# Kernel optimization log

Measured on AMD Instinct MI355X. Metric: run time of the kernel, lower is better.

The kernel has to match this reference:

```python
import jax, jax.numpy as jnp
import numpy as np

F = 128   # num_features
H = 128   # hidden sizes
U = 128   # u_size == out_size
N = 50000
E = 600000
B = 64
L = 4     # hops + 1 layers


def _scatter_mean(vals, idx, num_segments):
    s = jax.ops.segment_sum(vals, idx, num_segments=num_segments)
    cnt = jax.ops.segment_sum(jnp.ones((vals.shape[0],), vals.dtype), idx,
                              num_segments=num_segments)
    return s / jnp.maximum(cnt, 1.0)[:, None]


def setup_inputs() -> dict:
    key = jax.random.key(0)
    ks = jax.random.split(key, 20)
    x = jax.random.normal(ks[0], (N, F), jnp.float32)
    edge_index = jax.random.randint(ks[1], (2, E), 0, N, jnp.int64)
    u = jax.random.normal(ks[2], (B, U), jnp.float32)
    batch = jnp.sort(jax.random.randint(ks[3], (N,), 0, B, jnp.int64))
    sc = 0.05
    # stacked per-layer params (all layer dims identical since u_size==out_size)
    params = {
        'n1w1': jax.random.normal(ks[4], (L, F, H), jnp.float32) * sc,
        'n1b1': jnp.zeros((L, H), jnp.float32),
        'n1w2': jax.random.normal(ks[5], (L, H, H), jnp.float32) * sc,
        'n1b2': jnp.zeros((L, H), jnp.float32),
        'n2w1': jax.random.normal(ks[6], (L, F + H + U, H), jnp.float32) * sc,
        'n2b1': jnp.zeros((L, H), jnp.float32),
        'n2w2': jax.random.normal(ks[7], (L, H, F), jnp.float32) * sc,
        'n2b2': jnp.zeros((L, F), jnp.float32),
        'gw1': jax.random.normal(ks[8], (L, F + U, H), jnp.float32) * sc,
        'gb1': jnp.zeros((L, H), jnp.float32),
        'gw2': jax.random.normal(ks[9], (L, H, U), jnp.float32) * sc,
        'gb2': jnp.zeros((L, U), jnp.float32),
    }
    return dict(x=x, edge_index=edge_index, u=u, batch=batch, **params)


def reference(x, edge_index, u, batch,
              n1w1, n1b1, n1w2, n1b2, n2w1, n2b1, n2w2, n2b2,
              gw1, gb1, gw2, gb2):
    row, col = edge_index[0], edge_index[1]
    for l in range(L):
        # NodeModel
        m = jax.nn.relu(x[row] @ n1w1[l] + n1b1[l]) @ n1w2[l] + n1b2[l]  # [E,H]
        agg = _scatter_mean(m, col, N)                                    # [N,H]
        h = jnp.concatenate([x, agg, u[batch]], axis=1)                   # [N,F+H+U]
        x = jax.nn.relu(h @ n2w1[l] + n2b1[l]) @ n2w2[l] + n2b2[l]        # [N,F]
        # GlobalModel (uses updated x)
        g = jnp.concatenate([u, _scatter_mean(x, batch, B)], axis=1)      # [B,F+U]
        u = jax.nn.relu(g @ gw1[l] + gb1[l]) @ gw2[l] + gb2[l]            # [B,U]
    return (x, u)
```

## Files before the change

kernel.cpp:

```cpp
#include <hip/hip_runtime.h>

typedef __bf16 bf16;
typedef bf16 bf16x8 __attribute__((ext_vector_type(8)));
typedef bf16 bf16x4 __attribute__((ext_vector_type(4)));
typedef float floatx4 __attribute__((ext_vector_type(4)));

#define MFMA __builtin_amdgcn_mfma_f32_16x16x32_bf16


__global__ void hist_kernel(const int* __restrict__ ei, int* __restrict__ cnt, int E) {
  int e = blockIdx.x * blockDim.x + threadIdx.x;
  if (e < E) atomicAdd(&cnt[ei[E + e]], 1);
}

__global__ void gcnt_kernel(const int* __restrict__ batch, int* __restrict__ gcnt,
                            int N, int B) {
  const int b = threadIdx.x;
  if (b >= B) return;
  auto lb = [&](int v) {
    int lo = 0, hi = N;
    while (lo < hi) {
      const int mid = (lo + hi) >> 1;
      if (batch[mid] < v) lo = mid + 1; else hi = mid;
    }
    return lo;
  };
  gcnt[b] = lb(b + 1) - lb(b);
}

__global__ void scan1_kernel(const int* __restrict__ cnt, int* __restrict__ colptr,
                             int* __restrict__ rctr, int* __restrict__ btot, int n) {
  __shared__ int sd[256];
  const int tid = threadIdx.x;
  const int i0 = blockIdx.x * 2048 + tid * 8;
  int v[8];
  int tot = 0;
#pragma unroll
  for (int j = 0; j < 8; ++j) {
    const int i = i0 + j;
    v[j] = (i < n) ? cnt[i] : 0;
    tot += v[j];
  }
  sd[tid] = tot;
  __syncthreads();
  for (int off = 1; off < 256; off <<= 1) {
    const int t = (tid >= off) ? sd[tid - off] : 0;
    __syncthreads();
    sd[tid] += t;
    __syncthreads();
  }
  int excl = sd[tid] - tot;
#pragma unroll
  for (int j = 0; j < 8; ++j) {
    const int i = i0 + j;
    if (i < n) { colptr[i] = excl; rctr[i] = excl; }
    excl += v[j];
  }
  if (tid == 255) btot[blockIdx.x] = sd[255];
}

__global__ void scan2_kernel(int* __restrict__ colptr, int* __restrict__ rctr,
                             const int* __restrict__ btot, int n) {
  __shared__ int off_s;
  const int tid = threadIdx.x;
  if (blockIdx.x == 0) return;
  if (tid == 0) {
    int o = 0;
    for (int j = 0; j < (int)blockIdx.x; ++j) o += btot[j];
    off_s = o;
  }
  __syncthreads();
  const int off = off_s;
  const int i0 = blockIdx.x * 2048 + tid * 8;
#pragma unroll
  for (int j = 0; j < 8; ++j) {
    const int i = i0 + j;
    if (i < n) { colptr[i] += off; rctr[i] += off; }
  }
}

__global__ void place_kernel(const int* __restrict__ ei, int* __restrict__ rctr,
                             int* __restrict__ esrow, int E) {
  int e = blockIdx.x * blockDim.x + threadIdx.x;
  if (e >= E) return;
  const int r = ei[e];
  const int c = ei[E + e];
  const int p = atomicAdd(&rctr[c], 1);
  esrow[p] = r;
}

__global__ void wsplit_kernel(const float* __restrict__ src, bf16* __restrict__ dst,
                              int Ksrc, int K, int HH) {
  const int l = blockIdx.y;
  const int gid = blockIdx.x * blockDim.x + threadIdx.x;
  if (gid >= K * HH) return;
  const int h = gid / K, k = gid - h * K;
  const float v = src[(size_t)l * Ksrc * HH + (size_t)k * HH + h];
  const bf16 hi = (bf16)v;
  const bf16 lo = (bf16)(v - (float)hi);
  bf16* d = dst + (size_t)l * 2 * K * HH;
  d[(size_t)h * K + k] = hi;
  d[(size_t)K * HH + (size_t)h * K + k] = lo;
}

__global__ void xsplit_kernel(const float* __restrict__ x, bf16* __restrict__ xhi,
                              bf16* __restrict__ xlo, int n4) {
  const int i = blockIdx.x * 256 + threadIdx.x;
  if (i >= n4) return;
  const float4 v = ((const float4*)x)[i];
  bf16x4 h, l;
  const float vv[4] = {v.x, v.y, v.z, v.w};
#pragma unroll
  for (int r = 0; r < 4; ++r) {
    h[r] = (bf16)vv[r];
    l[r] = (bf16)(vv[r] - (float)h[r]);
  }
  *(bf16x4*)&xhi[(size_t)i * 4] = h;
  *(bf16x4*)&xlo[(size_t)i * 4] = l;
}

__global__ __launch_bounds__(256, 4)
void pnode_mfma(const bf16* __restrict__ xh, const bf16* __restrict__ xl,
                const bf16* __restrict__ w1t, const float* __restrict__ b1,
                const bf16* __restrict__ w2t, const float* __restrict__ b2,
                bf16* __restrict__ P, int N) {
  __shared__ __align__(16) bf16 R[2 * 64 * 136];

  const int tid = threadIdx.x;
  const int n0 = blockIdx.x * 64;
  const int wave = tid >> 6, lane = tid & 63, q = lane >> 4, lr = lane & 15;
  const int hbase = wave * 32;

  int nn[4];
#pragma unroll
  for (int nt = 0; nt < 4; ++nt) {
    int n = n0 + nt * 16 + lr;
    nn[nt] = (n > N - 1) ? (N - 1) : n;
  }

  const floatx4 zz = {0.f, 0.f, 0.f, 0.f};
  floatx4 acc[2][4];
#pragma unroll
  for (int mt = 0; mt < 2; ++mt)
#pragma unroll
    for (int nt = 0; nt < 4; ++nt) acc[mt][nt] = zz;

  {
    bf16x8 bh[2][4], bl[2][4];
#pragma unroll
    for (int nt = 0; nt < 4; ++nt) {
      const size_t off = (size_t)nn[nt] * 128 + q * 8;
      bh[0][nt] = *(const bf16x8*)(xh + off);
      bl[0][nt] = *(const bf16x8*)(xl + off);
    }
#pragma unroll
    for (int kc = 0; kc < 4; ++kc) {
      const int cur = kc & 1, nxt = cur ^ 1;
      if (kc < 3) {
#pragma unroll
        for (int nt = 0; nt < 4; ++nt) {
          const size_t off = (size_t)nn[nt] * 128 + (kc + 1) * 32 + q * 8;
          bh[nxt][nt] = *(const bf16x8*)(xh + off);
          bl[nxt][nt] = *(const bf16x8*)(xl + off);
        }
      }
      bf16x8 ah[2], al[2];
#pragma unroll
      for (int mt = 0; mt < 2; ++mt) {
        const bf16* wp = w1t + (size_t)(hbase + mt * 16 + lr) * 128 + kc * 32 + q * 8;
        ah[mt] = *(const bf16x8*)wp;
        al[mt] = *(const bf16x8*)(wp + 16384);
      }
#pragma unroll
      for (int nt = 0; nt < 4; ++nt)
#pragma unroll
        for (int mt = 0; mt < 2; ++mt) {
          acc[mt][nt] = MFMA(ah[mt], bh[cur][nt], acc[mt][nt], 0, 0, 0);
          acc[mt][nt] = MFMA(al[mt], bh[cur][nt], acc[mt][nt], 0, 0, 0);
          acc[mt][nt] = MFMA(ah[mt], bl[cur][nt], acc[mt][nt], 0, 0, 0);
        }
    }
  }

#pragma unroll
  for (int mt = 0; mt < 2; ++mt) {
    const int h0 = hbase + mt * 16 + q * 4;
    const float* bp = &b1[h0];
#pragma unroll
    for (int nt = 0; nt < 4; ++nt) {
      const int e = nt * 16 + lr;
      bf16x4 hh, ll;
#pragma unroll
      for (int r = 0; r < 4; ++r) {
        const float v = fmaxf(acc[mt][nt][r] + bp[r], 0.f);
        hh[r] = (bf16)v;
        ll[r] = (bf16)(v - (float)hh[r]);
      }
      *(bf16x4*)&R[e * 136 + h0] = hh;
      *(bf16x4*)&R[64 * 136 + e * 136 + h0] = ll;
      acc[mt][nt] = zz;
    }
  }
  __syncthreads();

#pragma unroll
  for (int ks = 0; ks < 4; ++ks) {
    bf16x8 ah[2], al[2], b2h[4], b2l[4];
#pragma unroll
    for (int mt = 0; mt < 2; ++mt) {
      const bf16* wp = w2t + (size_t)(hbase + mt * 16 + lr) * 128 + ks * 32 + q * 8;
      ah[mt] = *(const bf16x8*)wp;
      al[mt] = *(const bf16x8*)(wp + 16384);
    }
#pragma unroll
    for (int nt = 0; nt < 4; ++nt) {
      const bf16* hp = &R[(nt * 16 + lr) * 136 + ks * 32 + q * 8];
      b2h[nt] = *(const bf16x8*)hp;
      b2l[nt] = *(const bf16x8*)(hp + 64 * 136);
    }
#pragma unroll
    for (int nt = 0; nt < 4; ++nt)
#pragma unroll
      for (int mt = 0; mt < 2; ++mt) {
        acc[mt][nt] = MFMA(ah[mt], b2h[nt], acc[mt][nt], 0, 0, 0);
        acc[mt][nt] = MFMA(al[mt], b2h[nt], acc[mt][nt], 0, 0, 0);
        acc[mt][nt] = MFMA(ah[mt], b2l[nt], acc[mt][nt], 0, 0, 0);
      }
  }
  __syncthreads();

#pragma unroll
  for (int mt = 0; mt < 2; ++mt) {
    const int f0 = hbase + mt * 16 + q * 4;
    const float* bp = &b2[f0];
#pragma unroll
    for (int nt = 0; nt < 4; ++nt) {
      const int e = nt * 16 + lr;
      bf16x4 o;
#pragma unroll
      for (int r = 0; r < 4; ++r) o[r] = (bf16)(acc[mt][nt][r] + bp[r]);
      *(bf16x4*)&R[e * 136 + f0] = o;
    }
  }
  __syncthreads();
#pragma unroll
  for (int it = 0; it < 4; ++it) {
    const int idx = it * 256 + tid;
    const int row = idx >> 4;
    const int f8 = (idx & 15) * 8;
    const int n = n0 + row;
    if (n < N)
      *(bf16x8*)&P[(size_t)n * 128 + f8] = *(const bf16x8*)&R[row * 136 + f8];
  }
}

__global__ __launch_bounds__(256)
void agg_csr(const bf16* __restrict__ P, const int* __restrict__ colptr,
             const int* __restrict__ esrow,
             bf16* __restrict__ aggh, bf16* __restrict__ aggl, int N, int E) {
  const int f = threadIdx.x & 127;
  const int c = blockIdx.x * 2 + (threadIdx.x >> 7);
  if (c >= N) return;
  const int beg = colptr[c];
  const int end = (c == N - 1) ? E : colptr[c + 1];
  float sacc[4] = {0.f, 0.f, 0.f, 0.f};
  int e = beg;
  for (; e + 8 <= end; e += 8) {
    int r[8];
#pragma unroll
    for (int j = 0; j < 8; ++j) r[j] = esrow[e + j];
    float v[8];
#pragma unroll
    for (int j = 0; j < 8; ++j) v[j] = (float)P[(size_t)r[j] * 128 + f];
#pragma unroll
    for (int j = 0; j < 8; ++j) sacc[j & 3] += v[j];
  }
  const int rem = end - e;
  if (rem > 0) {
    int r[8];
#pragma unroll
    for (int j = 0; j < 8; ++j) r[j] = esrow[e + (j < rem ? j : 0)];
#pragma unroll
    for (int j = 0; j < 8; ++j) {
      const float v = (float)P[(size_t)r[j] * 128 + f];
      if (j < rem) sacc[j & 3] += v;
    }
  }
  const int cc = end - beg;
  const float val = ((sacc[0] + sacc[1]) + (sacc[2] + sacc[3])) /
                    (float)(cc > 1 ? cc : 1);
  const bf16 h = (bf16)val;
  aggh[(size_t)c * 128 + f] = h;
  aggl[(size_t)c * 128 + f] = (bf16)(val - (float)h);
}

__global__ __launch_bounds__(256, 4)
void node_p(bf16* xh, bf16* xl,
            const bf16* __restrict__ aggh, const bf16* __restrict__ aggl,
            const float* __restrict__ UW, const int* __restrict__ batch,
            const bf16* __restrict__ w1t, const bf16* __restrict__ w2t,
            const float* __restrict__ b2,
            const bf16* __restrict__ w1te, const float* __restrict__ b1e,
            const bf16* __restrict__ w2te, const float* __restrict__ b2e,
            bf16* __restrict__ Pout, float* __restrict__ gx,
            float* __restrict__ xout, int write_x, int has_next, int N) {
  __shared__ __align__(16) bf16 R[2 * 64 * 136];
  __shared__ int sbatch[64];

  const int tid = threadIdx.x;
  const int n0 = blockIdx.x * 64;
  const int wave = tid >> 6, lane = tid & 63, q = lane >> 4, lr = lane & 15;
  const int hbase = wave * 32;

  if (tid < 64) {
    int n = n0 + tid;
    sbatch[tid] = batch[(n > N - 1) ? (N - 1) : n];
  }

  int nn[4], ub[4];
#pragma unroll
  for (int nt = 0; nt < 4; ++nt) {
    int n = n0 + nt * 16 + lr;
    if (n > N - 1) n = N - 1;
    nn[nt] = n;
    ub[nt] = batch[n];
  }

  floatx4 acc[2][4];
#pragma unroll
  for (int mt = 0; mt < 2; ++mt)
#pragma unroll
    for (int nt = 0; nt < 4; ++nt)
      acc[mt][nt] = *(const floatx4*)&UW[(size_t)ub[nt] * 128 + hbase + mt * 16 + q * 4];

  {
    bf16x8 bh[2][4], bl[2][4];
    auto loadB = [&](int kc, int buf) {
#pragma unroll
      for (int nt = 0; nt < 4; ++nt) {
        if (kc < 4) {
          const size_t off = (size_t)nn[nt] * 128 + kc * 32 + q * 8;
          bh[buf][nt] = *(const bf16x8*)(xh + off);
          bl[buf][nt] = *(const bf16x8*)(xl + off);
        } else {
          const size_t off = (size_t)nn[nt] * 128 + (kc - 4) * 32 + q * 8;
          bh[buf][nt] = *(const bf16x8*)(aggh + off);
          bl[buf][nt] = *(const bf16x8*)(aggl + off);
        }
      }
    };
    loadB(0, 0);
#pragma unroll
    for (int kc = 0; kc < 8; ++kc) {
      const int cur = kc & 1, nxt = cur ^ 1;
      if (kc < 7) loadB(kc + 1, nxt);
      bf16x8 ah[2], al[2];
#pragma unroll
      for (int mt = 0; mt < 2; ++mt) {
        const bf16* wp = w1t + (size_t)(hbase + mt * 16 + lr) * 256 + kc * 32 + q * 8;
        ah[mt] = *(const bf16x8*)wp;
        al[mt] = *(const bf16x8*)(wp + 32768);
      }
#pragma unroll
      for (int nt = 0; nt < 4; ++nt)
#pragma unroll
        for (int mt = 0; mt < 2; ++mt) {
          acc[mt][nt] = MFMA(ah[mt], bh[cur][nt], acc[mt][nt], 0, 0, 0);
          acc[mt][nt] = MFMA(al[mt], bh[cur][nt], acc[mt][nt], 0, 0, 0);
          acc[mt][nt] = MFMA(ah[mt], bl[cur][nt], acc[mt][nt], 0, 0, 0);
        }
    }
  }

  const floatx4 zz = {0.f, 0.f, 0.f, 0.f};
#pragma unroll
  for (int mt = 0; mt < 2; ++mt) {
    const int h0 = hbase + mt * 16 + q * 4;
#pragma unroll
    for (int nt = 0; nt < 4; ++nt) {
      const int e = nt * 16 + lr;
      bf16x4 hh, ll;
#pragma unroll
      for (int r = 0; r < 4; ++r) {
        const float v = fmaxf(acc[mt][nt][r], 0.f);
        hh[r] = (bf16)v;
        ll[r] = (bf16)(v - (float)hh[r]);
      }
      *(bf16x4*)&R[e * 136 + h0] = hh;
      *(bf16x4*)&R[64 * 136 + e * 136 + h0] = ll;
      acc[mt][nt] = zz;
    }
  }
  __syncthreads();

#pragma unroll
  for (int ks = 0; ks < 4; ++ks) {
    bf16x8 ah[2], al[2], b2h[4], b2l[4];
#pragma unroll
    for (int mt = 0; mt < 2; ++mt) {
      const bf16* wp = w2t + (size_t)(hbase + mt * 16 + lr) * 128 + ks * 32 + q * 8;
      ah[mt] = *(const bf16x8*)wp;
      al[mt] = *(const bf16x8*)(wp + 16384);
    }
#pragma unroll
    for (int nt = 0; nt < 4; ++nt) {
      const bf16* hp = &R[(nt * 16 + lr) * 136 + ks * 32 + q * 8];
      b2h[nt] = *(const bf16x8*)hp;
      b2l[nt] = *(const bf16x8*)(hp + 64 * 136);
    }
#pragma unroll
    for (int nt = 0; nt < 4; ++nt)
#pragma unroll
      for (int mt = 0; mt < 2; ++mt) {
        acc[mt][nt] = MFMA(ah[mt], b2h[nt], acc[mt][nt], 0, 0, 0);
        acc[mt][nt] = MFMA(al[mt], b2h[nt], acc[mt][nt], 0, 0, 0);
        acc[mt][nt] = MFMA(ah[mt], b2l[nt], acc[mt][nt], 0, 0, 0);
      }
  }
  __syncthreads();

  float* Xt = (float*)&R[0];
#pragma unroll
  for (int mt = 0; mt < 2; ++mt) {
    const int f0 = hbase + mt * 16 + q * 4;
    const float* bp = &b2[f0];
#pragma unroll
    for (int nt = 0; nt < 4; ++nt) {
      const int e = nt * 16 + lr;
      const int n = n0 + e;
      float4 o;
      o.x = (n < N) ? acc[mt][nt][0] + bp[0] : 0.f;
      o.y = (n < N) ? acc[mt][nt][1] + bp[1] : 0.f;
      o.z = (n < N) ? acc[mt][nt][2] + bp[2] : 0.f;
      o.w = (n < N) ? acc[mt][nt][3] + bp[3] : 0.f;
      *(float4*)&Xt[e * 132 + f0] = o;
    }
  }
  __syncthreads();

  if (has_next) {
#pragma unroll
    for (int it = 0; it < 4; ++it) {
      const int idx = it * 256 + tid;
      const int row = idx >> 4;
      const int f8 = (idx & 15) * 8;
      const int n = n0 + row;
      if (n < N) {
        bf16x8 hh, ll;
#pragma unroll
        for (int j = 0; j < 8; ++j) {
          const float v = Xt[row * 132 + f8 + j];
          hh[j] = (bf16)v;
          ll[j] = (bf16)(v - (float)hh[j]);
        }
        *(bf16x8*)&xh[(size_t)n * 128 + f8] = hh;
        *(bf16x8*)&xl[(size_t)n * 128 + f8] = ll;
      }
    }
  }
  if (write_x) {
#pragma unroll
    for (int it = 0; it < 8; ++it) {
      const int idx = it * 256 + tid;
      const int row = idx >> 5;
      const int f4 = (idx & 31) * 4;
      const int n = n0 + row;
      if (n < N)
        *(float4*)&xout[(size_t)n * 128 + f4] = *(const float4*)&Xt[row * 132 + f4];
    }
  }

  {
    const int f = tid & 127;
    const int es = (tid >> 7) * 32;
    int cur = sbatch[es];
    float s = 0.f;
    for (int e = es; e < es + 32; ++e) {
      const int b = sbatch[e];
      const float v = Xt[e * 132 + f];
      if (b != cur) {
        atomicAdd(&gx[(size_t)cur * 128 + f], s);
        s = 0.f;
        cur = b;
      }
      s += v;
    }
    atomicAdd(&gx[(size_t)cur * 128 + f], s);
  }

  if (!has_next) return;

#pragma unroll
  for (int mt = 0; mt < 2; ++mt)
#pragma unroll
    for (int nt = 0; nt < 4; ++nt) acc[mt][nt] = zz;

#pragma unroll
  for (int kc = 0; kc < 4; ++kc) {
    bf16x8 ah[2], al[2], bh[4], bl[4];
#pragma unroll
    for (int mt = 0; mt < 2; ++mt) {
      const bf16* wp = w1te + (size_t)(hbase + mt * 16 + lr) * 128 + kc * 32 + q * 8;
      ah[mt] = *(const bf16x8*)wp;
      al[mt] = *(const bf16x8*)(wp + 16384);
    }
#pragma unroll
    for (int nt = 0; nt < 4; ++nt) {
      const float* xp = &Xt[(nt * 16 + lr) * 132 + kc * 32 + q * 8];
#pragma unroll
      for (int r = 0; r < 8; ++r) {
        const float v = xp[r];
        bh[nt][r] = (bf16)v;
        bl[nt][r] = (bf16)(v - (float)bh[nt][r]);
      }
    }
#pragma unroll
    for (int nt = 0; nt < 4; ++nt)
#pragma unroll
      for (int mt = 0; mt < 2; ++mt) {
        acc[mt][nt] = MFMA(ah[mt], bh[nt], acc[mt][nt], 0, 0, 0);
        acc[mt][nt] = MFMA(al[mt], bh[nt], acc[mt][nt], 0, 0, 0);
        acc[mt][nt] = MFMA(ah[mt], bl[nt], acc[mt][nt], 0, 0, 0);
      }
  }
  __syncthreads();

#pragma unroll
  for (int mt = 0; mt < 2; ++mt) {
    const int h0 = hbase + mt * 16 + q * 4;
    const float* bp = &b1e[h0];
#pragma unroll
    for (int nt = 0; nt < 4; ++nt) {
      const int e = nt * 16 + lr;
      bf16x4 hh, ll;
#pragma unroll
      for (int r = 0; r < 4; ++r) {
        const float v = fmaxf(acc[mt][nt][r] + bp[r], 0.f);
        hh[r] = (bf16)v;
        ll[r] = (bf16)(v - (float)hh[r]);
      }
      *(bf16x4*)&R[e * 136 + h0] = hh;
      *(bf16x4*)&R[64 * 136 + e * 136 + h0] = ll;
      acc[mt][nt] = zz;
    }
  }
  __syncthreads();

#pragma unroll
  for (int ks = 0; ks < 4; ++ks) {
    bf16x8 ah[2], al[2], b2h[4], b2l[4];
#pragma unroll
    for (int mt = 0; mt < 2; ++mt) {
      const bf16* wp = w2te + (size_t)(hbase + mt * 16 + lr) * 128 + ks * 32 + q * 8;
      ah[mt] = *(const bf16x8*)wp;
      al[mt] = *(const bf16x8*)(wp + 16384);
    }
#pragma unroll
    for (int nt = 0; nt < 4; ++nt) {
      const bf16* hp = &R[(nt * 16 + lr) * 136 + ks * 32 + q * 8];
      b2h[nt] = *(const bf16x8*)hp;
      b2l[nt] = *(const bf16x8*)(hp + 64 * 136);
    }
#pragma unroll
    for (int nt = 0; nt < 4; ++nt)
#pragma unroll
      for (int mt = 0; mt < 2; ++mt) {
        acc[mt][nt] = MFMA(ah[mt], b2h[nt], acc[mt][nt], 0, 0, 0);
        acc[mt][nt] = MFMA(al[mt], b2h[nt], acc[mt][nt], 0, 0, 0);
        acc[mt][nt] = MFMA(ah[mt], b2l[nt], acc[mt][nt], 0, 0, 0);
      }
  }
  __syncthreads();

#pragma unroll
  for (int mt = 0; mt < 2; ++mt) {
    const int f0 = hbase + mt * 16 + q * 4;
    const float* bp = &b2e[f0];
#pragma unroll
    for (int nt = 0; nt < 4; ++nt) {
      const int e = nt * 16 + lr;
      bf16x4 o;
#pragma unroll
      for (int r = 0; r < 4; ++r) o[r] = (bf16)(acc[mt][nt][r] + bp[r]);
      *(bf16x4*)&R[e * 136 + f0] = o;
    }
  }
  __syncthreads();
#pragma unroll
  for (int it = 0; it < 4; ++it) {
    const int idx = it * 256 + tid;
    const int row = idx >> 4;
    const int f8 = (idx & 15) * 8;
    const int n = n0 + row;
    if (n < N)
      *(bf16x8*)&Pout[(size_t)n * 128 + f8] = *(const bf16x8*)&R[row * 136 + f8];
  }
}

__global__ void uw_kernel(const float* __restrict__ u, const float* __restrict__ w1,
                          const float* __restrict__ b1, float* __restrict__ UW) {
  const int b = blockIdx.x, h = threadIdx.x;
  float s = b1[h];
#pragma unroll 8
  for (int k = 0; k < 128; ++k)
    s = fmaf(u[b * 128 + k], w1[(size_t)(256 + k) * 128 + h], s);
  UW[b * 128 + h] = s;
}

__global__ __launch_bounds__(128)
void gmlp_kernel(const float* __restrict__ uin, float* __restrict__ gx,
                 const int* __restrict__ gcnt,
                 const float* __restrict__ gw1, const float* __restrict__ gb1,
                 const float* __restrict__ gw2, const float* __restrict__ gb2,
                 float* __restrict__ uout,
                 const float* __restrict__ w1n_next,
                 const float* __restrict__ b1n_next,
                 float* __restrict__ UW, int has_next) {
  __shared__ float g[256];
  __shared__ float g1[128];
  const int b = blockIdx.x;
  const int t = threadIdx.x;
  const int c = gcnt[b];
  const float inv = 1.f / (float)(c > 1 ? c : 1);
  g[t] = uin[b * 128 + t];
  g[128 + t] = gx[b * 128 + t] * inv;
  gx[b * 128 + t] = 0.f;
  __syncthreads();
  float acc = gb1[t];
#pragma unroll 8
  for (int k = 0; k < 256; ++k) acc = fmaf(g[k], gw1[k * 128 + t], acc);
  g1[t] = fmaxf(acc, 0.f);
  __syncthreads();
  float acc2 = gb2[t];
#pragma unroll 8
  for (int k = 0; k < 128; ++k) acc2 = fmaf(g1[k], gw2[k * 128 + t], acc2);
  uout[b * 128 + t] = acc2;
  if (has_next) {
    __syncthreads();
    g[t] = acc2;
    __syncthreads();
    float s = b1n_next[t];
#pragma unroll 8
    for (int k = 0; k < 128; ++k)
      s = fmaf(g[k], w1n_next[(size_t)(256 + k) * 128 + t], s);
    UW[b * 128 + t] = s;
  }
}

extern "C" void kernel_launch(void* const* d_in, const int* in_sizes, int n_in,
                              void* d_out, int out_size, void* d_ws, size_t ws_size,
                              hipStream_t stream) {
  constexpr int N = 50000, E = 600000, B = 64, F = 128, L = 4;

  const float* x0    = (const float*)d_in[0];
  const int*   ei    = (const int*)  d_in[1];
  const float* u0    = (const float*)d_in[2];
  const int*   batch = (const int*)  d_in[3];
  const float* n1w1  = (const float*)d_in[4];
  const float* n1b1  = (const float*)d_in[5];
  const float* n1w2  = (const float*)d_in[6];
  const float* n1b2  = (const float*)d_in[7];
  const float* n2w1  = (const float*)d_in[8];
  const float* n2b1  = (const float*)d_in[9];
  const float* n2w2  = (const float*)d_in[10];
  const float* n2b2  = (const float*)d_in[11];
  const float* gw1   = (const float*)d_in[12];
  const float* gb1   = (const float*)d_in[13];
  const float* gw2   = (const float*)d_in[14];
  const float* gb2   = (const float*)d_in[15];
  float* out = (float*)d_out;

  char* p = (char*)d_ws;
  auto carve = [&](size_t bytes) -> void* {
    void* q = (void*)p;
    p += (bytes + 255) & ~(size_t)255;
    return q;
  };
  float* ubuf  = (float*)carve((size_t)B * F * 4);
  float* gx    = (float*)carve((size_t)B * F * 4);
  float* UW    = (float*)carve((size_t)B * F * 4);
  int*   cnt   = (int*)carve((size_t)N * 4);
  int*   colptr= (int*)carve((size_t)(N + 1) * 4);
  int*   rctr  = (int*)carve((size_t)N * 4);
  int*   gcnt  = (int*)carve((size_t)B * 4);
  int*   btot  = (int*)carve(32 * 4);
  int*   esrow = (int*)carve((size_t)E * 4);
  bf16*  xhi   = (bf16*)carve((size_t)N * F * 2);
  bf16*  xlo   = (bf16*)carve((size_t)N * F * 2);
  bf16*  P_a   = (bf16*)carve((size_t)N * F * 2);
  bf16*  P_b   = (bf16*)carve((size_t)N * F * 2);
  bf16*  aggh  = (bf16*)carve((size_t)N * F * 2);
  bf16*  aggl  = (bf16*)carve((size_t)N * F * 2);
  bf16*  w1t_e = (bf16*)carve((size_t)L * 2 * 128 * 128 * 2);
  bf16*  w2t_e = (bf16*)carve((size_t)L * 2 * 128 * 128 * 2);
  bf16*  w1t_n = (bf16*)carve((size_t)L * 2 * 256 * 128 * 2);
  bf16*  w2t_n = (bf16*)carve((size_t)L * 2 * 128 * 128 * 2);

  constexpr int SCAN_BLOCKS = (N + 2047) / 2048;

  hipMemsetAsync(cnt, 0, (size_t)N * 4, stream);
  hipMemsetAsync(gx, 0, (size_t)B * F * 4, stream);
  hist_kernel<<<(E + 255) / 256, 256, 0, stream>>>(ei, cnt, E);
  gcnt_kernel<<<1, 64, 0, stream>>>(batch, gcnt, N, B);
  scan1_kernel<<<SCAN_BLOCKS, 256, 0, stream>>>(cnt, colptr, rctr, btot, N);
  scan2_kernel<<<SCAN_BLOCKS, 256, 0, stream>>>(colptr, rctr, btot, N);
  place_kernel<<<(E + 255) / 256, 256, 0, stream>>>(ei, rctr, esrow, E);
  wsplit_kernel<<<dim3(64, L), 256, 0, stream>>>(n1w1, w1t_e, 128, 128, 128);
  wsplit_kernel<<<dim3(64, L), 256, 0, stream>>>(n1w2, w2t_e, 128, 128, 128);
  wsplit_kernel<<<dim3(128, L), 256, 0, stream>>>(n2w1, w1t_n, 384, 256, 128);
  wsplit_kernel<<<dim3(64, L), 256, 0, stream>>>(n2w2, w2t_n, 128, 128, 128);
  xsplit_kernel<<<(N * F / 4 + 255) / 256, 256, 0, stream>>>(x0, xhi, xlo, N * F / 4);
  uw_kernel<<<B, 128, 0, stream>>>(u0, n2w1, n2b1, UW);

  const int NB = (N + 63) / 64;
  pnode_mfma<<<NB, 256, 0, stream>>>(xhi, xlo, w1t_e, n1b1, w2t_e, n1b2, P_a, N);

  for (int l = 0; l < L; ++l) {
    const float* uin  = l ? ubuf : u0;
    float*       uout = (l == L - 1) ? out + (size_t)N * F : ubuf;
    const int    wx   = (l == L - 1) ? 1 : 0;
    const int    hn   = (l < L - 1) ? 1 : 0;
    const bf16*  Pin  = (l & 1) ? P_b : P_a;
    bf16*        Pout = (l & 1) ? P_a : P_b;
    const int    le   = hn ? (l + 1) : l;

    agg_csr<<<(N + 1) / 2, 256, 0, stream>>>(Pin, colptr, esrow, aggh, aggl, N, E);
    node_p<<<NB, 256, 0, stream>>>(
        xhi, xlo, aggh, aggl, UW, batch,
        w1t_n + (size_t)l * 65536, w2t_n + (size_t)l * 32768,
        n2b2 + l * 128,
        w1t_e + (size_t)le * 32768, n1b1 + le * 128,
        w2t_e + (size_t)le * 32768, n1b2 + le * 128,
        Pout, gx, out, wx, hn, N);
    gmlp_kernel<<<B, 128, 0, stream>>>(
        uin, gx, gcnt,
        gw1 + (size_t)l * 256 * 128, gb1 + l * 128,
        gw2 + (size_t)l * 128 * 128, gb2 + l * 128, uout,
        hn ? (n2w1 + (size_t)(l + 1) * 384 * 128) : n2w1,
        hn ? (n2b1 + (l + 1) * 128) : n2b1,
        UW, hn);
  }
}
```

Baseline: 794.5 us.

## Use 8 waves per MLP block and one wave per node in CSR aggregation

The fused node/edge MLP kernels now launch 512 threads per 64-node tile, with each wave owning 16 output columns instead of 32. This halves per-wave accumulators and removes the register double-buffering of B loads, raising occupancy. The CSR aggregation assigns one 64-lane wave per destination node and has each lane load a packed pair of bf16 features, so each block handles four nodes. The costs are redundant B-fragment loads across twice as many waves and the loss of explicit load prefetching.

```diff
diff --git a/kernel.cpp b/kernel.cpp
--- a/kernel.cpp
+++ b/kernel.cpp
@@ -3,9 +3,19 @@
 typedef __bf16 bf16;
 typedef bf16 bf16x8 __attribute__((ext_vector_type(8)));
 typedef bf16 bf16x4 __attribute__((ext_vector_type(4)));
+typedef bf16 bf16x2 __attribute__((ext_vector_type(2)));
 typedef float floatx4 __attribute__((ext_vector_type(4)));
 
 #define MFMA __builtin_amdgcn_mfma_f32_16x16x32_bf16
+
+__device__ __forceinline__ float bfhi_f(unsigned u) {
+  const unsigned x = u << 16;
+  return __builtin_bit_cast(float, x);
+}
+__device__ __forceinline__ float bflo_f(unsigned u) {
+  const unsigned x = u & 0xffff0000u;
+  return __builtin_bit_cast(float, x);
+}
 
 
 __global__ void hist_kernel(const int* __restrict__ ei, int* __restrict__ cnt, int E) {
@@ -119,7 +129,7 @@
   *(bf16x4*)&xlo[(size_t)i * 4] = l;
 }
 
-__global__ __launch_bounds__(256, 4)
+__global__ __launch_bounds__(512, 6)
 void pnode_mfma(const bf16* __restrict__ xh, const bf16* __restrict__ xl,
                 const bf16* __restrict__ w1t, const float* __restrict__ b1,
                 const bf16* __restrict__ w2t, const float* __restrict__ b2,
@@ -129,7 +139,7 @@
   const int tid = threadIdx.x;
   const int n0 = blockIdx.x * 64;
   const int wave = tid >> 6, lane = tid & 63, q = lane >> 4, lr = lane & 15;
-  const int hbase = wave * 32;
+  const int hbase = wave * 16;
 
   int nn[4];
 #pragma unroll
@@ -139,52 +149,32 @@
   }
 
   const floatx4 zz = {0.f, 0.f, 0.f, 0.f};
-  floatx4 acc[2][4];
-#pragma unroll
-  for (int mt = 0; mt < 2; ++mt)
-#pragma unroll
-    for (int nt = 0; nt < 4; ++nt) acc[mt][nt] = zz;
+  floatx4 acc[4];
+#pragma unroll
+  for (int nt = 0; nt < 4; ++nt) acc[nt] = zz;
+
+#pragma unroll
+  for (int kc = 0; kc < 4; ++kc) {
+    const bf16* wp = w1t + (size_t)(hbase + lr) * 128 + kc * 32 + q * 8;
+    const bf16x8 ah = *(const bf16x8*)wp;
+    const bf16x8 al = *(const bf16x8*)(wp + 16384);
+    bf16x8 bh[4], bl[4];
+#pragma unroll
+    for (int nt = 0; nt < 4; ++nt) {
+      const size_t off = (size_t)nn[nt] * 128 + kc * 32 + q * 8;
+      bh[nt] = *(const bf16x8*)(xh + off);
+      bl[nt] = *(const bf16x8*)(xl + off);
+    }
+#pragma unroll
+    for (int nt = 0; nt < 4; ++nt) {
+      acc[nt] = MFMA(ah, bh[nt], acc[nt], 0, 0, 0);
+      acc[nt] = MFMA(al, bh[nt], acc[nt], 0, 0, 0);
+      acc[nt] = MFMA(ah, bl[nt], acc[nt], 0, 0, 0);
+    }
+  }
 
   {
-    bf16x8 bh[2][4], bl[2][4];
-#pragma unroll
-    for (int nt = 0; nt < 4; ++nt) {
-      const size_t off = (size_t)nn[nt] * 128 + q * 8;
-      bh[0][nt] = *(const bf16x8*)(xh + off);
-      bl[0][nt] = *(const bf16x8*)(xl + off);
-    }
-#pragma unroll
-    for (int kc = 0; kc < 4; ++kc) {
-      const int cur = kc & 1, nxt = cur ^ 1;
-      if (kc < 3) {
-#pragma unroll
-        for (int nt = 0; nt < 4; ++nt) {
-          const size_t off = (size_t)nn[nt] * 128 + (kc + 1) * 32 + q * 8;
-          bh[nxt][nt] = *(const bf16x8*)(xh + off);
-          bl[nxt][nt] = *(const bf16x8*)(xl + off);
-        }
-      }
-      bf16x8 ah[2], al[2];
-#pragma unroll
-      for (int mt = 0; mt < 2; ++mt) {
-        const bf16* wp = w1t + (size_t)(hbase + mt * 16 + lr) * 128 + kc * 32 + q * 8;
-        ah[mt] = *(const bf16x8*)wp;
-        al[mt] = *(const bf16x8*)(wp + 16384);
-      }
-#pragma unroll
-      for (int nt = 0; nt < 4; ++nt)
-#pragma unroll
-        for (int mt = 0; mt < 2; ++mt) {
-          acc[mt][nt] = MFMA(ah[mt], bh[cur][nt], acc[mt][nt], 0, 0, 0);
-          acc[mt][nt] = MFMA(al[mt], bh[cur][nt], acc[mt][nt], 0, 0, 0);
-          acc[mt][nt] = MFMA(ah[mt], bl[cur][nt], acc[mt][nt], 0, 0, 0);
-        }
-    }
-  }
-
-#pragma unroll
-  for (int mt = 0; mt < 2; ++mt) {
-    const int h0 = hbase + mt * 16 + q * 4;
+    const int h0 = hbase + q * 4;
     const float* bp = &b1[h0];
 #pragma unroll
     for (int nt = 0; nt < 4; ++nt) {
@@ -192,26 +182,23 @@
       bf16x4 hh, ll;
 #pragma unroll
       for (int r = 0; r < 4; ++r) {
-        const float v = fmaxf(acc[mt][nt][r] + bp[r], 0.f);
+        const float v = fmaxf(acc[nt][r] + bp[r], 0.f);
         hh[r] = (bf16)v;
         ll[r] = (bf16)(v - (float)hh[r]);
       }
       *(bf16x4*)&R[e * 136 + h0] = hh;
       *(bf16x4*)&R[64 * 136 + e * 136 + h0] = ll;
-      acc[mt][nt] = zz;
+      acc[nt] = zz;
     }
   }
   __syncthreads();
 
 #pragma unroll
   for (int ks = 0; ks < 4; ++ks) {
-    bf16x8 ah[2], al[2], b2h[4], b2l[4];
-#pragma unroll
-    for (int mt = 0; mt < 2; ++mt) {
-      const bf16* wp = w2t + (size_t)(hbase + mt * 16 + lr) * 128 + ks * 32 + q * 8;
-      ah[mt] = *(const bf16x8*)wp;
-      al[mt] = *(const bf16x8*)(wp + 16384);
-    }
+    const bf16* wp = w2t + (size_t)(hbase + lr) * 128 + ks * 32 + q * 8;
+    const bf16x8 ah = *(const bf16x8*)wp;
+    const bf16x8 al = *(const bf16x8*)(wp + 16384);
+    bf16x8 b2h[4], b2l[4];
 #pragma unroll
     for (int nt = 0; nt < 4; ++nt) {
       const bf16* hp = &R[(nt * 16 + lr) * 136 + ks * 32 + q * 8];
@@ -219,33 +206,30 @@
       b2l[nt] = *(const bf16x8*)(hp + 64 * 136);
     }
 #pragma unroll
-    for (int nt = 0; nt < 4; ++nt)
-#pragma unroll
-      for (int mt = 0; mt < 2; ++mt) {
-        acc[mt][nt] = MFMA(ah[mt], b2h[nt], acc[mt][nt], 0, 0, 0);
-        acc[mt][nt] = MFMA(al[mt], b2h[nt], acc[mt][nt], 0, 0, 0);
-        acc[mt][nt] = MFMA(ah[mt], b2l[nt], acc[mt][nt], 0, 0, 0);
-      }
-  }
-  __syncthreads();
-
-#pragma unroll
-  for (int mt = 0; mt < 2; ++mt) {
-    const int f0 = hbase + mt * 16 + q * 4;
+    for (int nt = 0; nt < 4; ++nt) {
+      acc[nt] = MFMA(ah, b2h[nt], acc[nt], 0, 0, 0);
+      acc[nt] = MFMA(al, b2h[nt], acc[nt], 0, 0, 0);
+      acc[nt] = MFMA(ah, b2l[nt], acc[nt], 0, 0, 0);
+    }
+  }
+  __syncthreads();
+
+  {
+    const int f0 = hbase + q * 4;
     const float* bp = &b2[f0];
 #pragma unroll
     for (int nt = 0; nt < 4; ++nt) {
       const int e = nt * 16 + lr;
       bf16x4 o;
 #pragma unroll
-      for (int r = 0; r < 4; ++r) o[r] = (bf16)(acc[mt][nt][r] + bp[r]);
+      for (int r = 0; r < 4; ++r) o[r] = (bf16)(acc[nt][r] + bp[r]);
       *(bf16x4*)&R[e * 136 + f0] = o;
     }
   }
   __syncthreads();
 #pragma unroll
-  for (int it = 0; it < 4; ++it) {
-    const int idx = it * 256 + tid;
+  for (int it = 0; it < 2; ++it) {
+    const int idx = it * 512 + tid;
     const int row = idx >> 4;
     const int f8 = (idx & 15) * 8;
     const int n = n0 + row;
@@ -254,47 +238,61 @@
   }
 }
 
-__global__ __launch_bounds__(256)
+__global__ __launch_bounds__(256, 8)
 void agg_csr(const bf16* __restrict__ P, const int* __restrict__ colptr,
              const int* __restrict__ esrow,
              bf16* __restrict__ aggh, bf16* __restrict__ aggl, int N, int E) {
-  const int f = threadIdx.x & 127;
-  const int c = blockIdx.x * 2 + (threadIdx.x >> 7);
+  const int lane = threadIdx.x & 63;
+  const int c = blockIdx.x * 4 + (threadIdx.x >> 6);
   if (c >= N) return;
   const int beg = colptr[c];
   const int end = (c == N - 1) ? E : colptr[c + 1];
-  float sacc[4] = {0.f, 0.f, 0.f, 0.f};
+  float s0[4] = {0.f, 0.f, 0.f, 0.f};
+  float s1[4] = {0.f, 0.f, 0.f, 0.f};
   int e = beg;
   for (; e + 8 <= end; e += 8) {
     int r[8];
 #pragma unroll
     for (int j = 0; j < 8; ++j) r[j] = esrow[e + j];
-    float v[8];
-#pragma unroll
-    for (int j = 0; j < 8; ++j) v[j] = (float)P[(size_t)r[j] * 128 + f];
-#pragma unroll
-    for (int j = 0; j < 8; ++j) sacc[j & 3] += v[j];
+    unsigned v[8];
+#pragma unroll
+    for (int j = 0; j < 8; ++j)
+      v[j] = *(const unsigned*)&P[(size_t)r[j] * 128 + lane * 2];
+#pragma unroll
+    for (int j = 0; j < 8; ++j) {
+      s0[j & 3] += bfhi_f(v[j]);
+      s1[j & 3] += bflo_f(v[j]);
+    }
   }
   const int rem = end - e;
   if (rem > 0) {
     int r[8];
 #pragma unroll
     for (int j = 0; j < 8; ++j) r[j] = esrow[e + (j < rem ? j : 0)];
+    unsigned v[8];
+#pragma unroll
+    for (int j = 0; j < 8; ++j)
+      v[j] = *(const unsigned*)&P[(size_t)r[j] * 128 + lane * 2];
 #pragma unroll
     for (int j = 0; j < 8; ++j) {
-      const float v = (float)P[(size_t)r[j] * 128 + f];
-      if (j < rem) sacc[j & 3] += v;
+      if (j < rem) {
+        s0[j & 3] += bfhi_f(v[j]);
+        s1[j & 3] += bflo_f(v[j]);
+      }
     }
   }
   const int cc = end - beg;
-  const float val = ((sacc[0] + sacc[1]) + (sacc[2] + sacc[3])) /
-                    (float)(cc > 1 ? cc : 1);
-  const bf16 h = (bf16)val;
-  aggh[(size_t)c * 128 + f] = h;
-  aggl[(size_t)c * 128 + f] = (bf16)(val - (float)h);
-}
-
-__global__ __launch_bounds__(256, 4)
+  const float inv = 1.f / (float)(cc > 1 ? cc : 1);
+  const float v0 = ((s0[0] + s0[1]) + (s0[2] + s0[3])) * inv;
+  const float v1 = ((s1[0] + s1[1]) + (s1[2] + s1[3])) * inv;
+  bf16x2 h, l;
+  h[0] = (bf16)v0;  l[0] = (bf16)(v0 - (float)h[0]);
+  h[1] = (bf16)v1;  l[1] = (bf16)(v1 - (float)h[1]);
+  *(bf16x2*)&aggh[(size_t)c * 128 + lane * 2] = h;
+  *(bf16x2*)&aggl[(size_t)c * 128 + lane * 2] = l;
+}
+
+__global__ __launch_bounds__(512, 6)
 void node_p(bf16* xh, bf16* xl,
             const bf16* __restrict__ aggh, const bf16* __restrict__ aggl,
             const float* __restrict__ UW, const int* __restrict__ batch,
@@ -310,7 +308,7 @@
   const int tid = threadIdx.x;
   const int n0 = blockIdx.x * 64;
   const int wave = tid >> 6, lane = tid & 63, q = lane >> 4, lr = lane & 15;
-  const int hbase = wave * 32;
+  const int hbase = wave * 16;
 
   if (tid < 64) {
     int n = n0 + tid;
@@ -326,82 +324,63 @@
     ub[nt] = batch[n];
   }
 
-  floatx4 acc[2][4];
-#pragma unroll
-  for (int mt = 0; mt < 2; ++mt)
-#pragma unroll
-    for (int nt = 0; nt < 4; ++nt)
-      acc[mt][nt] = *(const floatx4*)&UW[(size_t)ub[nt] * 128 + hbase + mt * 16 + q * 4];
-
+  floatx4 acc[4];
+#pragma unroll
+  for (int nt = 0; nt < 4; ++nt)
+    acc[nt] = *(const floatx4*)&UW[(size_t)ub[nt] * 128 + hbase + q * 4];
+
+#pragma unroll
+  for (int kc = 0; kc < 8; ++kc) {
+    const bf16* wp = w1t + (size_t)(hbase + lr) * 256 + kc * 32 + q * 8;
+    const bf16x8 ah = *(const bf16x8*)wp;
+    const bf16x8 al = *(const bf16x8*)(wp + 32768);
+    bf16x8 bh[4], bl[4];
+#pragma unroll
+    for (int nt = 0; nt < 4; ++nt) {
+      if (kc < 4) {
+        const size_t off = (size_t)nn[nt] * 128 + kc * 32 + q * 8;
+        bh[nt] = *(const bf16x8*)(xh + off);
+        bl[nt] = *(const bf16x8*)(xl + off);
+      } else {
+        const size_t off = (size_t)nn[nt] * 128 + (kc - 4) * 32 + q * 8;
+        bh[nt] = *(const bf16x8*)(aggh + off);
+        bl[nt] = *(const bf16x8*)(aggl + off);
+      }
+    }
+#pragma unroll
+    for (int nt = 0; nt < 4; ++nt) {
+      acc[nt] = MFMA(ah, bh[nt], acc[nt], 0, 0, 0);
+      acc[nt] = MFMA(al, bh[nt], acc[nt], 0, 0, 0);
+      acc[nt] = MFMA(ah, bl[nt], acc[nt], 0, 0, 0);
+    }
+  }
+
+  const floatx4 zz = {0.f, 0.f, 0.f, 0.f};
   {
-    bf16x8 bh[2][4], bl[2][4];
-    auto loadB = [&](int kc, int buf) {
-#pragma unroll
-      for (int nt = 0; nt < 4; ++nt) {
-        if (kc < 4) {
-          const size_t off = (size_t)nn[nt] * 128 + kc * 32 + q * 8;
-          bh[buf][nt] = *(const bf16x8*)(xh + off);
-          bl[buf][nt] = *(const bf16x8*)(xl + off);
-        } else {
-          const size_t off = (size_t)nn[nt] * 128 + (kc - 4) * 32 + q * 8;
-          bh[buf][nt] = *(const bf16x8*)(aggh + off);
-          bl[buf][nt] = *(const bf16x8*)(aggl + off);
-        }
-      }
-    };
-    loadB(0, 0);
-#pragma unroll
-    for (int kc = 0; kc < 8; ++kc) {
-      const int cur = kc & 1, nxt = cur ^ 1;
-      if (kc < 7) loadB(kc + 1, nxt);
-      bf16x8 ah[2], al[2];
-#pragma unroll
-      for (int mt = 0; mt < 2; ++mt) {
-        const bf16* wp = w1t + (size_t)(hbase + mt * 16 + lr) * 256 + kc * 32 + q * 8;
-        ah[mt] = *(const bf16x8*)wp;
-        al[mt] = *(const bf16x8*)(wp + 32768);
-      }
-#pragma unroll
-      for (int nt = 0; nt < 4; ++nt)
-#pragma unroll
-        for (int mt = 0; mt < 2; ++mt) {
-          acc[mt][nt] = MFMA(ah[mt], bh[cur][nt], acc[mt][nt], 0, 0, 0);
-          acc[mt][nt] = MFMA(al[mt], bh[cur][nt], acc[mt][nt], 0, 0, 0);
-          acc[mt][nt] = MFMA(ah[mt], bl[cur][nt], acc[mt][nt], 0, 0, 0);
-        }
-    }
-  }
-
-  const floatx4 zz = {0.f, 0.f, 0.f, 0.f};
-#pragma unroll
-  for (int mt = 0; mt < 2; ++mt) {
-    const int h0 = hbase + mt * 16 + q * 4;
+    const int h0 = hbase + q * 4;
 #pragma unroll
     for (int nt = 0; nt < 4; ++nt) {
       const int e = nt * 16 + lr;
       bf16x4 hh, ll;
 #pragma unroll
       for (int r = 0; r < 4; ++r) {
-        const float v = fmaxf(acc[mt][nt][r], 0.f);
+        const float v = fmaxf(acc[nt][r], 0.f);
         hh[r] = (bf16)v;
         ll[r] = (bf16)(v - (float)hh[r]);
       }
       *(bf16x4*)&R[e * 136 + h0] = hh;
       *(bf16x4*)&R[64 * 136 + e * 136 + h0] = ll;
-      acc[mt][nt] = zz;
+      acc[nt] = zz;
     }
   }
   __syncthreads();
 
 #pragma unroll
   for (int ks = 0; ks < 4; ++ks) {
-    bf16x8 ah[2], al[2], b2h[4], b2l[4];
-#pragma unroll
-    for (int mt = 0; mt < 2; ++mt) {
-      const bf16* wp = w2t + (size_t)(hbase + mt * 16 + lr) * 128 + ks * 32 + q * 8;
-      ah[mt] = *(const bf16x8*)wp;
-      al[mt] = *(const bf16x8*)(wp + 16384);
-    }
+    const bf16* wp = w2t + (size_t)(hbase + lr) * 128 + ks * 32 + q * 8;
+    const bf16x8 ah = *(const bf16x8*)wp;
+    const bf16x8 al = *(const bf16x8*)(wp + 16384);
+    bf16x8 b2h[4], b2l[4];
 #pragma unroll
     for (int nt = 0; nt < 4; ++nt) {
       const bf16* hp = &R[(nt * 16 + lr) * 136 + ks * 32 + q * 8];
@@ -409,30 +388,27 @@
       b2l[nt] = *(const bf16x8*)(hp + 64 * 136);
     }
 #pragma unroll
-    for (int nt = 0; nt < 4; ++nt)
-#pragma unroll
-      for (int mt = 0; mt < 2; ++mt) {
-        acc[mt][nt] = MFMA(ah[mt], b2h[nt], acc[mt][nt], 0, 0, 0);
-        acc[mt][nt] = MFMA(al[mt], b2h[nt], acc[mt][nt], 0, 0, 0);
-        acc[mt][nt] = MFMA(ah[mt], b2l[nt], acc[mt][nt], 0, 0, 0);
-      }
+    for (int nt = 0; nt < 4; ++nt) {
+      acc[nt] = MFMA(ah, b2h[nt], acc[nt], 0, 0, 0);
+      acc[nt] = MFMA(al, b2h[nt], acc[nt], 0, 0, 0);
+      acc[nt] = MFMA(ah, b2l[nt], acc[nt], 0, 0, 0);
+    }
   }
   __syncthreads();
 
   float* Xt = (float*)&R[0];
-#pragma unroll
-  for (int mt = 0; mt < 2; ++mt) {
-    const int f0 = hbase + mt * 16 + q * 4;
+  {
+    const int f0 = hbase + q * 4;
     const float* bp = &b2[f0];
 #pragma unroll
     for (int nt = 0; nt < 4; ++nt) {
       const int e = nt * 16 + lr;
       const int n = n0 + e;
       float4 o;
-      o.x = (n < N) ? acc[mt][nt][0] + bp[0] : 0.f;
-      o.y = (n < N) ? acc[mt][nt][1] + bp[1] : 0.f;
-      o.z = (n < N) ? acc[mt][nt][2] + bp[2] : 0.f;
-      o.w = (n < N) ? acc[mt][nt][3] + bp[3] : 0.f;
+      o.x = (n < N) ? acc[nt][0] + bp[0] : 0.f;
+      o.y = (n < N) ? acc[nt][1] + bp[1] : 0.f;
+      o.z = (n < N) ? acc[nt][2] + bp[2] : 0.f;
+      o.w = (n < N) ? acc[nt][3] + bp[3] : 0.f;
       *(float4*)&Xt[e * 132 + f0] = o;
     }
   }
@@ -440,8 +416,8 @@
 
   if (has_next) {
 #pragma unroll
-    for (int it = 0; it < 4; ++it) {
-      const int idx = it * 256 + tid;
+    for (int it = 0; it < 2; ++it) {
+      const int idx = it * 512 + tid;
       const int row = idx >> 4;
       const int f8 = (idx & 15) * 8;
       const int n = n0 + row;
@@ -460,8 +436,8 @@
   }
   if (write_x) {
 #pragma unroll
-    for (int it = 0; it < 8; ++it) {
-      const int idx = it * 256 + tid;
+    for (int it = 0; it < 4; ++it) {
+      const int idx = it * 512 + tid;
       const int row = idx >> 5;
       const int f4 = (idx & 31) * 4;
       const int n = n0 + row;
@@ -472,10 +448,10 @@
 
   {
     const int f = tid & 127;
-    const int es = (tid >> 7) * 32;
+    const int es = (tid >> 7) * 16;
     int cur = sbatch[es];
     float s = 0.f;
-    for (int e = es; e < es + 32; ++e) {
+    for (int e = es; e < es + 16; ++e) {
       const int b = sbatch[e];
       const float v = Xt[e * 132 + f];
       if (b != cur) {
@@ -491,19 +467,14 @@
   if (!has_next) return;
 
 #pragma unroll
-  for (int mt = 0; mt < 2; ++mt)
-#pragma unroll
-    for (int nt = 0; nt < 4; ++nt) acc[mt][nt] = zz;
+  for (int nt = 0; nt < 4; ++nt) acc[nt] = zz;
 
 #pragma unroll
   for (int kc = 0; kc < 4; ++kc) {
-    bf16x8 ah[2], al[2], bh[4], bl[4];
-#pragma unroll
-    for (int mt = 0; mt < 2; ++mt) {
-      const bf16* wp = w1te + (size_t)(hbase + mt * 16 + lr) * 128 + kc * 32 + q * 8;
-      ah[mt] = *(const bf16x8*)wp;
-      al[mt] = *(const bf16x8*)(wp + 16384);
-    }
+    const bf16* wp = w1te + (size_t)(hbase + lr) * 128 + kc * 32 + q * 8;
+    const bf16x8 ah = *(const bf16x8*)wp;
+    const bf16x8 al = *(const bf16x8*)(wp + 16384);
+    bf16x8 bh[4], bl[4];
 #pragma unroll
     for (int nt = 0; nt < 4; ++nt) {
       const float* xp = &Xt[(nt * 16 + lr) * 132 + kc * 32 + q * 8];
@@ -515,19 +486,16 @@
       }
     }
 #pragma unroll
-    for (int nt = 0; nt < 4; ++nt)
-#pragma unroll
-      for (int mt = 0; mt < 2; ++mt) {
-        acc[mt][nt] = MFMA(ah[mt], bh[nt], acc[mt][nt], 0, 0, 0);
-        acc[mt][nt] = MFMA(al[mt], bh[nt], acc[mt][nt], 0, 0, 0);
-        acc[mt][nt] = MFMA(ah[mt], bl[nt], acc[mt][nt], 0, 0, 0);
-      }
-  }
-  __syncthreads();
-
-#pragma unroll
-  for (int mt = 0; mt < 2; ++mt) {
-    const int h0 = hbase + mt * 16 + q * 4;
+    for (int nt = 0; nt < 4; ++nt) {
+      acc[nt] = MFMA(ah, bh[nt], acc[nt], 0, 0, 0);
+      acc[nt] = MFMA(al, bh[nt], acc[nt], 0, 0, 0);
+      acc[nt] = MFMA(ah, bl[nt], acc[nt], 0, 0, 0);
+    }
+  }
+  __syncthreads();
+
+  {
+    const int h0 = hbase + q * 4;
     const float* bp = &b1e[h0];
 #pragma unroll
     for (int nt = 0; nt < 4; ++nt) {
@@ -535,26 +503,23 @@
       bf16x4 hh, ll;
 #pragma unroll
       for (int r = 0; r < 4; ++r) {
-        const float v = fmaxf(acc[mt][nt][r] + bp[r], 0.f);
+        const float v = fmaxf(acc[nt][r] + bp[r], 0.f);
         hh[r] = (bf16)v;
         ll[r] = (bf16)(v - (float)hh[r]);
       }
       *(bf16x4*)&R[e * 136 + h0] = hh;
       *(bf16x4*)&R[64 * 136 + e * 136 + h0] = ll;
-      acc[mt][nt] = zz;
+      acc[nt] = zz;
     }
   }
   __syncthreads();
 
 #pragma unroll
   for (int ks = 0; ks < 4; ++ks) {
-    bf16x8 ah[2], al[2], b2h[4], b2l[4];
-#pragma unroll
-    for (int mt = 0; mt < 2; ++mt) {
-      const bf16* wp = w2te + (size_t)(hbase + mt * 16 + lr) * 128 + ks * 32 + q * 8;
-      ah[mt] = *(const bf16x8*)wp;
-      al[mt] = *(const bf16x8*)(wp + 16384);
-    }
+    const bf16* wp = w2te + (size_t)(hbase + lr) * 128 + ks * 32 + q * 8;
+    const bf16x8 ah = *(const bf16x8*)wp;
+    const bf16x8 al = *(const bf16x8*)(wp + 16384);
+    bf16x8 b2h[4], b2l[4];
 #pragma unroll
     for (int nt = 0; nt < 4; ++nt) {
       const bf16* hp = &R[(nt * 16 + lr) * 136 + ks * 32 + q * 8];
@@ -562,33 +527,30 @@
       b2l[nt] = *(const bf16x8*)(hp + 64 * 136);
     }
 #pragma unroll
-    for (int nt = 0; nt < 4; ++nt)
-#pragma unroll
-      for (int mt = 0; mt < 2; ++mt) {
-        acc[mt][nt] = MFMA(ah[mt], b2h[nt], acc[mt][nt], 0, 0, 0);
-        acc[mt][nt] = MFMA(al[mt], b2h[nt], acc[mt][nt], 0, 0, 0);
-        acc[mt][nt] = MFMA(ah[mt], b2l[nt], acc[mt][nt], 0, 0, 0);
-      }
-  }
-  __syncthreads();
-
-#pragma unroll
-  for (int mt = 0; mt < 2; ++mt) {
-    const int f0 = hbase + mt * 16 + q * 4;
+    for (int nt = 0; nt < 4; ++nt) {
+      acc[nt] = MFMA(ah, b2h[nt], acc[nt], 0, 0, 0);
+      acc[nt] = MFMA(al, b2h[nt], acc[nt], 0, 0, 0);
+      acc[nt] = MFMA(ah, b2l[nt], acc[nt], 0, 0, 0);
+    }
+  }
+  __syncthreads();
+
+  {
+    const int f0 = hbase + q * 4;
     const float* bp = &b2e[f0];
 #pragma unroll
     for (int nt = 0; nt < 4; ++nt) {
       const int e = nt * 16 + lr;
       bf16x4 o;
 #pragma unroll
-      for (int r = 0; r < 4; ++r) o[r] = (bf16)(acc[mt][nt][r] + bp[r]);
+      for (int r = 0; r < 4; ++r) o[r] = (bf16)(acc[nt][r] + bp[r]);
       *(bf16x4*)&R[e * 136 + f0] = o;
     }
   }
   __syncthreads();
 #pragma unroll
-  for (int it = 0; it < 4; ++it) {
-    const int idx = it * 256 + tid;
+  for (int it = 0; it < 2; ++it) {
+    const int idx = it * 512 + tid;
     const int row = idx >> 4;
     const int f8 = (idx & 15) * 8;
     const int n = n0 + row;
@@ -713,7 +675,7 @@
   uw_kernel<<<B, 128, 0, stream>>>(u0, n2w1, n2b1, UW);
 
   const int NB = (N + 63) / 64;
-  pnode_mfma<<<NB, 256, 0, stream>>>(xhi, xlo, w1t_e, n1b1, w2t_e, n1b2, P_a, N);
+  pnode_mfma<<<NB, 512, 0, stream>>>(xhi, xlo, w1t_e, n1b1, w2t_e, n1b2, P_a, N);
 
   for (int l = 0; l < L; ++l) {
     const float* uin  = l ? ubuf : u0;
@@ -724,8 +686,8 @@
     bf16*        Pout = (l & 1) ? P_a : P_b;
     const int    le   = hn ? (l + 1) : l;
 
-    agg_csr<<<(N + 1) / 2, 256, 0, stream>>>(Pin, colptr, esrow, aggh, aggl, N, E);
-    node_p<<<NB, 256, 0, stream>>>(
+    agg_csr<<<(N + 3) / 4, 256, 0, stream>>>(Pin, colptr, esrow, aggh, aggl, N, E);
+    node_p<<<NB, 512, 0, stream>>>(
         xhi, xlo, aggh, aggl, UW, batch,
         w1t_n + (size_t)l * 65536, w2t_n + (size_t)l * 32768,
         n2b2 + l * 128,
```

After: 829.1 us. 4.3% more time.
